# Kernel optimization log

Hardware: AMD Instinct MI355X
Metric: run time of the kernel (lower is better)

The kernel has to match this reference:

```python
import jax, jax.numpy as jnp
import numpy as np

NUM_HEADS = 16
NUM_BUCKETS = 32
MAX_DISTANCE = 128


def _rel_bucket(rel):
    # bidirectional T5-style relative position bucketing
    nb = NUM_BUCKETS // 2
    ret = (rel > 0).astype(jnp.int32) * nb
    n = jnp.abs(rel)
    max_exact = nb // 2
    is_small = n < max_exact
    safe = jnp.maximum(n, 1).astype(jnp.float32)
    large = max_exact + (jnp.log(safe / max_exact) / np.log(MAX_DISTANCE / max_exact) * (nb - max_exact)).astype(jnp.int32)
    large = jnp.minimum(large, nb - 1)
    return ret + jnp.where(is_small, n, large)


def setup_inputs() -> dict:
    key = jax.random.key(0)
    ks = jax.random.split(key, 12)
    S, B, E = 1024, 4, 1024
    D = E // NUM_HEADS
    s = 0.02
    return {
        "query": jax.random.normal(ks[0], (S, B, E), jnp.float32),
        "q_w": jax.random.normal(ks[1], (E, E), jnp.float32) * s,
        "q_b": jnp.zeros((E,), jnp.float32),
        "k_w": jax.random.normal(ks[2], (E, E), jnp.float32) * s,
        "k_b": jnp.zeros((E,), jnp.float32),
        "v_w": jax.random.normal(ks[3], (E, E), jnp.float32) * s,
        "v_b": jnp.zeros((E,), jnp.float32),
        "out_w": jax.random.normal(ks[4], (E, E), jnp.float32) * s,
        "out_b": jnp.zeros((E,), jnp.float32),
        "rel_emb": jax.random.normal(ks[5], (NUM_BUCKETS, NUM_HEADS), jnp.float32) * s,
        "grep_w": jax.random.normal(ks[6], (8, D), jnp.float32) * s,
        "grep_b": jnp.zeros((8,), jnp.float32),
        "grep_a": jnp.ones((NUM_HEADS,), jnp.float32),
    }


def reference(query, q_w, q_b, k_w, k_b, v_w, v_b, out_w, out_b, rel_emb, grep_w, grep_b, grep_a):
    S, B, E = query.shape
    H = NUM_HEADS
    D = E // H
    scaling = D ** -0.5

    q = (query @ q_w.T + q_b) * scaling  # scaling applied before gating, as in WavLM
    k = query @ k_w.T + k_b
    v = query @ v_w.T + v_b

    def split(x):  # (S,B,E) -> (B,H,S,D)
        return x.reshape(S, B, H, D).transpose(1, 2, 0, 3)

    q4, k4, v4 = split(q), split(k), split(v)

    attn = jnp.einsum('bhqd,bhkd->bhqk', q4, k4)  # (B,H,S,S)

    pos = jnp.arange(S)
    bucket = _rel_bucket(pos[None, :] - pos[:, None])  # (S,S)
    pbias = rel_emb[bucket].transpose(2, 0, 1)          # (H,S,S)

    # GRU-gated relative position scaling
    g = jnp.einsum('bhsd,ed->bhse', q4, grep_w) + grep_b      # (B,H,S,8)
    g = jax.nn.sigmoid(g.reshape(B, H, S, 2, 4).sum(-1))     # (B,H,S,2)
    gate_a, gate_b = g[..., 0], g[..., 1]
    gate = gate_a * (gate_b * grep_a[None, :, None] - 1.0) + 2.0  # (B,H,S)

    attn = attn + gate[..., None] * pbias[None]
    probs = jax.nn.softmax(attn, axis=-1)
    ctx = jnp.einsum('bhqk,bhkd->bhqd', probs, v4)  # (B,H,S,D)
    out = ctx.transpose(2, 0, 1, 3).reshape(S, B, E) @ out_w.T + out_b
    return out
```

## Files before the change

kernel.cpp:

```cpp
#include <hip/hip_runtime.h>
#include <stdint.h>


typedef short bf16x8 __attribute__((ext_vector_type(8)));
typedef float f32x4 __attribute__((ext_vector_type(4)));

#define MFMA_BF16(a, b, c) __builtin_amdgcn_mfma_f32_16x16x32_bf16((a), (b), (c), 0, 0, 0)

#define LOG2E 1.44269504088896f
#define LN2 0.693147180559945f

__device__ __forceinline__ unsigned short f2bf(float x) {
  union { float f; unsigned u; } v; v.f = x;
  unsigned r = v.u + 0x7fffu + ((v.u >> 16) & 1u);
  return (unsigned short)(r >> 16);
}
__device__ __forceinline__ float bf2f(unsigned short u) {
  union { unsigned u; float f; } v; v.u = ((unsigned)u) << 16;
  return v.f;
}

__device__ __forceinline__ void gload_lds16(const void* g, void* l) {
  __builtin_amdgcn_global_load_lds(
      (const __attribute__((address_space(1))) unsigned int*)g,
      (__attribute__((address_space(3))) unsigned int*)l, 16, 0, 0);
}

__device__ __forceinline__ int swz(int row) { return (row ^ (row >> 2)) & 3; }

__global__ __launch_bounds__(256) void prep_kernel(
    const float* __restrict__ query, const float* __restrict__ q_w,
    const float* __restrict__ k_w, const float* __restrict__ v_w,
    const float* __restrict__ out_w, const float* __restrict__ rel_emb,
    unsigned short* __restrict__ q_bf, unsigned short* __restrict__ wq,
    unsigned short* __restrict__ wk, unsigned short* __restrict__ wv,
    unsigned short* __restrict__ ohi, unsigned short* __restrict__ olo,
    float* __restrict__ bias_d) {
  int i = blockIdx.x * 256 + threadIdx.x;
  if (i < 4194304) {
    int e = i & 1023;
    int sb = i >> 10;
    int s = sb >> 2, b = sb & 3;
    q_bf[((size_t)(b * 1024 + s) << 10) | e] = f2bf(query[i]);
  } else if (i < 5242880) {
    int j = i - 4194304;
    wq[j] = f2bf(q_w[j]);
    wk[j] = f2bf(k_w[j]);
    wv[j] = f2bf(v_w[j]);
    float x = out_w[j];
    unsigned short h = f2bf(x);
    ohi[j] = h;
    olo[j] = f2bf(x - bf2f(h));
  } else {
    int idx = i - 5242880;
    if (idx >= 2048) return;
    if (idx == 2047) {
#pragma unroll
      for (int h = 0; h < 16; ++h) bias_d[h * 2048 + idx] = 0.f;
      return;
    }
    int rel = idx - 1023;
    int n = rel < 0 ? -rel : rel;
    int ret = rel > 0 ? 16 : 0;
    int bucket;
    if (n < 8) {
      bucket = ret + n;
    } else {
      int large = 8 + (int)(logf((float)n / 8.0f) / logf(16.0f) * 8.0f);
      if (large > 15) large = 15;
      bucket = ret + large;
    }
#pragma unroll
    for (int h = 0; h < 16; ++h)
      bias_d[h * 2048 + idx] = rel_emb[bucket * 16 + h] * LOG2E;
  }
}

__global__ __launch_bounds__(256, 3) void qkv_gemm_kernel(
    const unsigned short* __restrict__ A, const unsigned short* __restrict__ Wq,
    const unsigned short* __restrict__ Wk, const unsigned short* __restrict__ Wv,
    const float* __restrict__ qb, const float* __restrict__ kb, const float* __restrict__ vb,
    unsigned short* __restrict__ qh,
    unsigned short* __restrict__ kh,
    unsigned short* __restrict__ vT)
{
  __shared__ __align__(16) char smem[32768];
  const int tid = threadIdx.x, lane = tid & 63;
  const int wv_ = tid >> 6;
  const int nt = blockIdx.x;
  const int mt = blockIdx.y;
  const int mat = nt >> 3;
  const unsigned short* W = mat == 0 ? Wq : (mat == 1 ? Wk : Wv);
  const int n0 = (nt & 7) * 128;
  const int m0 = mt * 128;
  const int moff = (wv_ & 1) * 64;
  const int noff = (wv_ >> 1) * 64;

  f32x4 acc[4][4] = {};
  const char* Ab = (const char*)A;
  const char* Wb = (const char*)W;

  int st_row[2], st_g[2];
#pragma unroll
  for (int c = 0; c < 2; ++c) {
    int o = c * 4096 + tid * 16;
    int row = o >> 6, p = (o >> 4) & 3;
    st_row[c] = row;
    st_g[c] = p ^ swz(row);
  }

#define QKV_STAGE(kt, buf)                                                     \
  {                                                                            \
    char* bb = smem + (buf)*16384;                                             \
    _Pragma("unroll") for (int c = 0; c < 2; ++c) {                            \
      int o = c * 4096 + tid * 16;                                             \
      size_t ga = (size_t)(m0 + st_row[c]) * 2048 + (size_t)(kt)*64 + st_g[c] * 16; \
      size_t gb = (size_t)(n0 + st_row[c]) * 2048 + (size_t)(kt)*64 + st_g[c] * 16; \
      gload_lds16(Ab + ga, bb + o);                                            \
      gload_lds16(Wb + gb, bb + 8192 + o);                                     \
    }                                                                          \
  }

  QKV_STAGE(0, 0);
  for (int kt = 0; kt < 32; ++kt) {
    __syncthreads();
    const char* base = smem + (kt & 1) * 16384;
    if (kt < 31) QKV_STAGE(kt + 1, (kt + 1) & 1);

    bf16x8 af[4], bfr[4];
#pragma unroll
    for (int i = 0; i < 4; ++i) {
      int ra = moff + i * 16 + (lane & 15);
      int rb = noff + i * 16 + (lane & 15);
      int q = lane >> 4;
      af[i] = *(const bf16x8*)(base + ra * 64 + (q ^ swz(ra)) * 16);
      bfr[i] = *(const bf16x8*)(base + 8192 + rb * 64 + (q ^ swz(rb)) * 16);
    }
#pragma unroll
    for (int i = 0; i < 4; ++i)
#pragma unroll
      for (int j = 0; j < 4; ++j) acc[i][j] = MFMA_BF16(af[i], bfr[j], acc[i][j]);
  }
#undef QKV_STAGE

  const int bidx = m0 >> 10;
  const int s00 = (m0 & 1023) + moff + ((lane >> 4) << 2);
  const int c0 = n0 + noff + (lane & 15);
  if (mat < 2) {
    const float* barr = mat == 0 ? qb : kb;
    unsigned short* dst = mat == 0 ? qh : kh;
    const float scale = mat == 0 ? (0.125f * LOG2E) : 1.0f;
#pragma unroll
    for (int j = 0; j < 4; ++j) {
      int col = c0 + j * 16;
      int hh = col >> 6, dd = col & 63;
      float bias = barr[col];
#pragma unroll
      for (int i = 0; i < 4; ++i)
#pragma unroll
        for (int r = 0; r < 4; ++r) {
          int s = s00 + i * 16 + r;
          dst[((size_t)(bidx * 16 + hh) * 1024 + s) * 64 + dd] =
              f2bf((acc[i][j][r] + bias) * scale);
        }
    }
  } else {
#pragma unroll
    for (int j = 0; j < 4; ++j) {
      int col = c0 + j * 16;
      int hh = col >> 6, dd = col & 63;
      float bias = vb[col];
#pragma unroll
      for (int i = 0; i < 4; ++i) {
        int s = s00 + i * 16;
        ushort4 pk;
        pk.x = f2bf(acc[i][j][0] + bias);
        pk.y = f2bf(acc[i][j][1] + bias);
        pk.z = f2bf(acc[i][j][2] + bias);
        pk.w = f2bf(acc[i][j][3] + bias);
        *(ushort4*)&vT[((size_t)(bidx * 16 + hh) * 64 + dd) * 1024 + s] = pk;
      }
    }
  }
}

__global__ __launch_bounds__(256) void gate_kernel(const unsigned short* __restrict__ qh,
                                                   const float* __restrict__ grep_w,
                                                   const float* __restrict__ grep_b,
                                                   const float* __restrict__ grep_a,
                                                   float* __restrict__ gate) {
  __shared__ float gw[512];
  __shared__ float gbb[8];
  __shared__ float gaa[16];
  int tid = threadIdx.x;
  for (int i = tid; i < 512; i += 256) gw[i] = grep_w[i];
  if (tid < 8) gbb[tid] = grep_b[tid];
  if (tid < 16) gaa[tid] = grep_a[tid];
  __syncthreads();
  int idx = blockIdx.x * 256 + tid;
  int h = (idx >> 10) & 15;
  const unsigned short* qrow = qh + (size_t)idx * 64;
  float a[8] = {0.f, 0.f, 0.f, 0.f, 0.f, 0.f, 0.f, 0.f};
#pragma unroll
  for (int c = 0; c < 8; ++c) {
    bf16x8 v = *(const bf16x8*)(qrow + c * 8);
#pragma unroll
    for (int jj = 0; jj < 8; ++jj) {
      float qv = bf2f((unsigned short)v[jj]);
      int d = c * 8 + jj;
#pragma unroll
      for (int e = 0; e < 8; ++e) a[e] += qv * gw[e * 64 + d];
    }
  }
  float sa = (a[0] + a[1] + a[2] + a[3]) * LN2 + gbb[0] + gbb[1] + gbb[2] + gbb[3];
  float sb = (a[4] + a[5] + a[6] + a[7]) * LN2 + gbb[4] + gbb[5] + gbb[6] + gbb[7];
  float siga = 1.f / (1.f + __expf(-sa));
  float sigb = 1.f / (1.f + __expf(-sb));
  gate[idx] = siga * (sigb * gaa[h] - 1.f) + 2.f;
}

__global__ __launch_bounds__(512, 6) void attn_kernel(
    const unsigned short* __restrict__ qh, const unsigned short* __restrict__ kh,
    const unsigned short* __restrict__ vT, const float* __restrict__ gate,
    const float* __restrict__ bias_d, unsigned short* __restrict__ ctx_hi,
    unsigned short* __restrict__ ctx_lo) {
  __shared__ __align__(16) char smem[53760];
  const int tid = threadIdx.x, lane = tid & 63, w = tid >> 6;
  const int bh = blockIdx.x;
  const int h = bh & 15;
  const int s0 = blockIdx.y * 128;
  const int sqb = s0 + w * 16;
  const int q15 = lane & 15, quad = lane >> 4, q7 = lane & 7;

  float* biasw = (float*)(smem + 49152);
  if (tid < 288)
    ((float4*)biasw)[tid] = ((const float4*)(bias_d + h * 2048 + (896 - s0)))[tid];

  const char* kbase = (const char*)(kh + (size_t)bh * 65536);
  const char* vbase = (const char*)(vT + (size_t)bh * 65536);

  const int o = tid * 16;
  const int srow = o >> 7;
  const int sg = ((o >> 4) & 7) ^ (srow & 7);
  const size_t koff = (size_t)srow * 128 + sg * 16;
  const size_t voff = (size_t)srow * 2048 + sg * 16;

  gload_lds16(kbase + koff, smem + o);
  gload_lds16(vbase + voff, smem + 16384 + o);

  const unsigned short* qbase = qh + ((size_t)bh * 1024 + sqb + q15) * 64 + (quad << 3);
  bf16x8 qf0 = *(const bf16x8*)(qbase);
  bf16x8 qf1 = *(const bf16x8*)(qbase + 32);

  const int sq = sqb + q15;
  const float gate_lane = gate[bh * 1024 + sq];

  unsigned short* psrow = (unsigned short*)(smem + 32768 + w * 2048) + q15 * 64;

  float l_run = 0.f;
  f32x4 acc_o[4] = {};

  for (int kc = 0; kc < 16; ++kc) {
    __syncthreads();
    const char* Kc = smem + (kc & 1) * 8192;
    const char* Vc = smem + 16384 + (kc & 1) * 8192;
    if (kc < 15) {
      int nb = (kc + 1) & 1;
      gload_lds16(kbase + (size_t)(kc + 1) * 8192 + koff, smem + nb * 8192 + o);
      gload_lds16(vbase + (size_t)(kc + 1) * 128 + voff, smem + 16384 + nb * 8192 + o);
    }

    const int boff = kc * 64 - sq + s0 + 127 + (quad << 2);
    float ps = 0.f;
#pragma unroll
    for (int t = 0; t < 4; ++t) {
      f32x4 sacc = {};
      int key = t * 16 + q15;
#pragma unroll
      for (int dc = 0; dc < 2; ++dc) {
        int c16 = dc * 4 + quad;
        bf16x8 ak = *(const bf16x8*)(Kc + key * 128 + ((c16 ^ (key & 7)) << 4));
        sacc = MFMA_BF16(ak, dc ? qf1 : qf0, sacc);
      }
      float p0 = __builtin_exp2f(__builtin_fmaf(gate_lane, biasw[boff + t * 16 + 0], sacc[0]));
      float p1 = __builtin_exp2f(__builtin_fmaf(gate_lane, biasw[boff + t * 16 + 1], sacc[1]));
      float p2 = __builtin_exp2f(__builtin_fmaf(gate_lane, biasw[boff + t * 16 + 2], sacc[2]));
      float p3 = __builtin_exp2f(__builtin_fmaf(gate_lane, biasw[boff + t * 16 + 3], sacc[3]));
      ps += (p0 + p1) + (p2 + p3);
      ushort4 pk;
      pk.x = f2bf(p0); pk.y = f2bf(p1); pk.z = f2bf(p2); pk.w = f2bf(p3);
      int c = t * 4 + quad;
      int pc = (c >> 1) ^ q7;
      *(ushort4*)(psrow + pc * 8 + (c & 1) * 4) = pk;
    }
    l_run += ps;

#pragma unroll
    for (int ch = 0; ch < 2; ++ch) {
      int j = (ch * 4 + quad) ^ q7;
      bf16x8 pb = *(const bf16x8*)(psrow + j * 8);
#pragma unroll
      for (int t = 0; t < 4; ++t) {
        int d = t * 16 + q15;
        int c16 = ch * 4 + quad;
        bf16x8 av = *(const bf16x8*)(Vc + d * 128 + ((c16 ^ (d & 7)) << 4));
        acc_o[t] = MFMA_BF16(av, pb, acc_o[t]);
      }
    }
  }

  l_run += __shfl_xor(l_run, 16, 64);
  l_run += __shfl_xor(l_run, 32, 64);
  const float inv = 1.0f / l_run;

  __syncthreads();
  float* Ot = (float*)smem;
  {
    float* ow = Ot + (w * 16 + q15) * 65;
#pragma unroll
    for (int t = 0; t < 4; ++t)
#pragma unroll
      for (int r = 0; r < 4; ++r) ow[t * 16 + (quad << 2) + r] = acc_o[t][r] * inv;
  }
  __syncthreads();
  {
    int row = tid >> 2, dg = tid & 3;
    int s = s0 + row;
    const float* src = Ot + row * 65 + dg * 16;
    unsigned short hibuf[16], lobuf[16];
#pragma unroll
    for (int j = 0; j < 16; ++j) {
      float v = src[j];
      unsigned short hu = f2bf(v);
      hibuf[j] = hu;
      lobuf[j] = f2bf(v - bf2f(hu));
    }
    size_t base = (size_t)(s * 4 + (bh >> 4)) * 1024 + h * 64 + dg * 16;
#pragma unroll
    for (int half = 0; half < 2; ++half) {
      *(uint4*)(ctx_hi + base + half * 8) = *(const uint4*)(hibuf + half * 8);
      *(uint4*)(ctx_lo + base + half * 8) = *(const uint4*)(lobuf + half * 8);
    }
  }
}

__global__ __launch_bounds__(256, 3) void outproj_kernel(
    const unsigned short* __restrict__ Ahi, const unsigned short* __restrict__ Alo,
    const unsigned short* __restrict__ Bhi, const unsigned short* __restrict__ Blo,
    const float* __restrict__ ob, float* __restrict__ out) {
  __shared__ __align__(16) char smem[49152];
  const int tid = threadIdx.x, lane = tid & 63, wv_ = tid >> 6;
  const int q15 = lane & 15, quad = lane >> 4;
  const int n0 = blockIdx.x * 128;
  const int m0 = blockIdx.y * 64;
  const int moff = (wv_ & 1) * 32;
  const int noff = (wv_ >> 1) * 64;

  const int oa = tid * 16;
  const int ra_ = oa >> 6;
  const int ga_ = (((oa >> 4) & 3) ^ swz(ra_)) << 4;
  int rb_[2], gb_[2], obo_[2];
#pragma unroll
  for (int c = 0; c < 2; ++c) {
    int ob2 = c * 4096 + tid * 16;
    obo_[c] = ob2;
    rb_[c] = ob2 >> 6;
    gb_[c] = (((ob2 >> 4) & 3) ^ swz(rb_[c])) << 4;
  }

#define OP_STAGE(kt, buf)                                                        \
  {                                                                              \
    char* bb = smem + (buf)*24576;                                               \
    size_t ga = (size_t)(m0 + ra_) * 2048 + (size_t)(kt)*64 + ga_;               \
    gload_lds16((const char*)Ahi + ga, bb + oa);                                 \
    gload_lds16((const char*)Alo + ga, bb + 4096 + oa);                          \
    _Pragma("unroll") for (int c = 0; c < 2; ++c) {                              \
      size_t gb = (size_t)(n0 + rb_[c]) * 2048 + (size_t)(kt)*64 + gb_[c];       \
      gload_lds16((const char*)Bhi + gb, bb + 8192 + obo_[c]);                   \
      gload_lds16((const char*)Blo + gb, bb + 16384 + obo_[c]);                  \
    }                                                                            \
  }

  f32x4 acc[2][4] = {};
  OP_STAGE(0, 0);
  for (int kt = 0; kt < 32; ++kt) {
    __syncthreads();
    const char* base = smem + (kt & 1) * 24576;
    if (kt < 31) OP_STAGE(kt + 1, (kt + 1) & 1);

    bf16x8 ah[2], al[2], bhf[4], blf[4];
#pragma unroll
    for (int i = 0; i < 2; ++i) {
      int ra = moff + i * 16 + q15;
      int pa = (quad ^ swz(ra)) << 4;
      ah[i] = *(const bf16x8*)(base + ra * 64 + pa);
      al[i] = *(const bf16x8*)(base + 4096 + ra * 64 + pa);
    }
#pragma unroll
    for (int j = 0; j < 4; ++j) {
      int rb = noff + j * 16 + q15;
      int pb = (quad ^ swz(rb)) << 4;
      bhf[j] = *(const bf16x8*)(base + 8192 + rb * 64 + pb);
      blf[j] = *(const bf16x8*)(base + 16384 + rb * 64 + pb);
    }
#pragma unroll
    for (int i = 0; i < 2; ++i)
#pragma unroll
      for (int j = 0; j < 4; ++j) {
        f32x4 t = MFMA_BF16(al[i], bhf[j], acc[i][j]);
        t = MFMA_BF16(ah[i], blf[j], t);
        acc[i][j] = MFMA_BF16(ah[i], bhf[j], t);
      }
  }
#undef OP_STAGE

  const int rr0 = m0 + moff + (quad << 2);
  const int c0 = n0 + noff + q15;
#pragma unroll
  for (int j = 0; j < 4; ++j) {
    int col = c0 + j * 16;
    float bias = ob[col];
#pragma unroll
    for (int i = 0; i < 2; ++i)
#pragma unroll
      for (int r = 0; r < 4; ++r)
        out[(size_t)(rr0 + i * 16 + r) * 1024 + col] = acc[i][j][r] + bias;
  }
}

extern "C" void kernel_launch(void* const* d_in, const int* in_sizes, int n_in,
                              void* d_out, int out_size, void* d_ws, size_t ws_size,
                              hipStream_t stream) {
  const float* query = (const float*)d_in[0];
  const float* q_w = (const float*)d_in[1];
  const float* q_b = (const float*)d_in[2];
  const float* k_w = (const float*)d_in[3];
  const float* k_b = (const float*)d_in[4];
  const float* v_w = (const float*)d_in[5];
  const float* v_b = (const float*)d_in[6];
  const float* out_w = (const float*)d_in[7];
  const float* out_b = (const float*)d_in[8];
  const float* rel_emb = (const float*)d_in[9];
  const float* grep_w = (const float*)d_in[10];
  const float* grep_b = (const float*)d_in[11];
  const float* grep_a = (const float*)d_in[12];
  float* out = (float*)d_out;

  const size_t MB = 1u << 20;
  char* ws = (char*)d_ws;
  unsigned short* q_bf = (unsigned short*)(ws);
  unsigned short* wq_bf = (unsigned short*)(ws + 8 * MB);
  unsigned short* wk_bf = (unsigned short*)(ws + 10 * MB);
  unsigned short* wv_bf = (unsigned short*)(ws + 12 * MB);
  unsigned short* ow_hi = (unsigned short*)(ws + 14 * MB);
  unsigned short* ow_lo = (unsigned short*)(ws + 16 * MB);
  unsigned short* qhp = (unsigned short*)(ws + 18 * MB);
  unsigned short* khp = (unsigned short*)(ws + 26 * MB);
  unsigned short* vTp = (unsigned short*)(ws + 34 * MB);
  unsigned short* ctxh = (unsigned short*)(ws + 42 * MB);
  unsigned short* ctxl = (unsigned short*)(ws + 50 * MB);
  float* gatep = (float*)(ws + 58 * MB);
  float* biasp = (float*)(ws + 58 * MB + 256 * 1024);

  prep_kernel<<<20488, 256, 0, stream>>>(query, q_w, k_w, v_w, out_w, rel_emb, q_bf, wq_bf,
                                         wk_bf, wv_bf, ow_hi, ow_lo, biasp);
  qkv_gemm_kernel<<<dim3(24, 32), 256, 0, stream>>>(q_bf, wq_bf, wk_bf, wv_bf, q_b, k_b, v_b,
                                                    qhp, khp, vTp);
  gate_kernel<<<256, 256, 0, stream>>>(qhp, grep_w, grep_b, grep_a, gatep);
  attn_kernel<<<dim3(64, 8), 512, 0, stream>>>(qhp, khp, vTp, gatep, biasp, ctxh, ctxl);
  outproj_kernel<<<dim3(8, 64), 256, 0, stream>>>(ctxh, ctxl, ow_hi, ow_lo, out_b, out);
}
```

Measured before the change: 211.4 us.

## Use fp16 single-pass out-projection and 32x32 MFMA attention with bf16 bias

The out-projection drops the hi/lo bf16 split (three MFMAs per tile) in favor of a single fp16 MFMA on fp16 context and weights, which halves LDS and global traffic for that GEMM. The attention kernel moves to 256-thread blocks with 32x32x16 MFMAs, where each wave handles 32 query rows. The relative bias is stored as bf16 in two parity-shifted LDS copies so it can be read as packed 32-bit pairs. This trades numerical precision in the output projection and bias for fewer instructions and less memory traffic, and occupancy may change.

```diff
diff --git a/kernel.cpp b/kernel.cpp
--- a/kernel.cpp
+++ b/kernel.cpp
@@ -3,9 +3,13 @@
 
 
 typedef short bf16x8 __attribute__((ext_vector_type(8)));
+typedef _Float16 f16x8 __attribute__((ext_vector_type(8)));
 typedef float f32x4 __attribute__((ext_vector_type(4)));
+typedef float f32x16 __attribute__((ext_vector_type(16)));
 
 #define MFMA_BF16(a, b, c) __builtin_amdgcn_mfma_f32_16x16x32_bf16((a), (b), (c), 0, 0, 0)
+#define MFMA_F16(a, b, c) __builtin_amdgcn_mfma_f32_16x16x32_f16((a), (b), (c), 0, 0, 0)
+#define MFMA32_BF16(a, b, c) __builtin_amdgcn_mfma_f32_32x32x16_bf16((a), (b), (c), 0, 0, 0)
 
 #define LOG2E 1.44269504088896f
 #define LN2 0.693147180559945f
@@ -17,6 +21,18 @@
 }
 __device__ __forceinline__ float bf2f(unsigned short u) {
   union { unsigned u; float f; } v; v.u = ((unsigned)u) << 16;
+  return v.f;
+}
+__device__ __forceinline__ unsigned short f2h(float x) {
+  union { _Float16 h; unsigned short u; } v; v.h = (_Float16)x;
+  return v.u;
+}
+__device__ __forceinline__ float u32lo_bf(unsigned u) {
+  union { unsigned u; float f; } v; v.u = u << 16;
+  return v.f;
+}
+__device__ __forceinline__ float u32hi_bf(unsigned u) {
+  union { unsigned u; float f; } v; v.u = u & 0xffff0000u;
   return v.f;
 }
 
@@ -34,8 +50,8 @@
     const float* __restrict__ out_w, const float* __restrict__ rel_emb,
     unsigned short* __restrict__ q_bf, unsigned short* __restrict__ wq,
     unsigned short* __restrict__ wk, unsigned short* __restrict__ wv,
-    unsigned short* __restrict__ ohi, unsigned short* __restrict__ olo,
-    float* __restrict__ bias_d) {
+    unsigned short* __restrict__ ow_h,
+    unsigned short* __restrict__ bias_hd) {
   int i = blockIdx.x * 256 + threadIdx.x;
   if (i < 4194304) {
     int e = i & 1023;
@@ -47,16 +63,13 @@
     wq[j] = f2bf(q_w[j]);
     wk[j] = f2bf(k_w[j]);
     wv[j] = f2bf(v_w[j]);
-    float x = out_w[j];
-    unsigned short h = f2bf(x);
-    ohi[j] = h;
-    olo[j] = f2bf(x - bf2f(h));
+    ow_h[j] = f2h(out_w[j]);
   } else {
     int idx = i - 5242880;
-    if (idx >= 2048) return;
-    if (idx == 2047) {
-#pragma unroll
-      for (int h = 0; h < 16; ++h) bias_d[h * 2048 + idx] = 0.f;
+    if (idx >= 2056) return;
+    if (idx >= 2047) {
+#pragma unroll
+      for (int h = 0; h < 16; ++h) bias_hd[h * 2056 + idx] = 0;
       return;
     }
     int rel = idx - 1023;
@@ -72,7 +85,7 @@
     }
 #pragma unroll
     for (int h = 0; h < 16; ++h)
-      bias_d[h * 2048 + idx] = rel_emb[bucket * 16 + h] * LOG2E;
+      bias_hd[h * 2056 + idx] = f2bf(rel_emb[bucket * 16 + h] * LOG2E);
   }
 }
 
@@ -219,46 +232,58 @@
   gate[idx] = siga * (sigb * gaa[h] - 1.f) + 2.f;
 }
 
-__global__ __launch_bounds__(512, 6) void attn_kernel(
+__global__ __launch_bounds__(256, 2) void attn_kernel(
     const unsigned short* __restrict__ qh, const unsigned short* __restrict__ kh,
     const unsigned short* __restrict__ vT, const float* __restrict__ gate,
-    const float* __restrict__ bias_d, unsigned short* __restrict__ ctx_hi,
-    unsigned short* __restrict__ ctx_lo) {
-  __shared__ __align__(16) char smem[53760];
+    const unsigned short* __restrict__ bias_hd, unsigned short* __restrict__ ctx) {
+  __shared__ __align__(16) char smem[55808];
   const int tid = threadIdx.x, lane = tid & 63, w = tid >> 6;
   const int bh = blockIdx.x;
   const int h = bh & 15;
-  const int s0 = blockIdx.y * 128;
-  const int sqb = s0 + w * 16;
-  const int q15 = lane & 15, quad = lane >> 4, q7 = lane & 7;
-
-  float* biasw = (float*)(smem + 49152);
-  if (tid < 288)
-    ((float4*)biasw)[tid] = ((const float4*)(bias_d + h * 2048 + (896 - s0)))[tid];
+  const int qs0 = blockIdx.y * 128;
+  const int q31 = lane & 31, hb = lane >> 5, q7 = q31 & 7;
+  const int sq = qs0 + w * 32 + q31;
+
+  unsigned short* bc0 = (unsigned short*)(smem + 51200);
+  unsigned short* bc1 = (unsigned short*)(smem + 53504);
+  {
+    const unsigned short* gb = bias_hd + h * 2056 + (896 - qs0);
+    for (int i = tid; i < 1152; i += 256) {
+      bc0[i] = gb[i];
+      bc1[i] = gb[i + 1];
+    }
+  }
 
   const char* kbase = (const char*)(kh + (size_t)bh * 65536);
   const char* vbase = (const char*)(vT + (size_t)bh * 65536);
 
-  const int o = tid * 16;
-  const int srow = o >> 7;
-  const int sg = ((o >> 4) & 7) ^ (srow & 7);
-  const size_t koff = (size_t)srow * 128 + sg * 16;
-  const size_t voff = (size_t)srow * 2048 + sg * 16;
-
-  gload_lds16(kbase + koff, smem + o);
-  gload_lds16(vbase + voff, smem + 16384 + o);
-
-  const unsigned short* qbase = qh + ((size_t)bh * 1024 + sqb + q15) * 64 + (quad << 3);
-  bf16x8 qf0 = *(const bf16x8*)(qbase);
-  bf16x8 qf1 = *(const bf16x8*)(qbase + 32);
-
-  const int sq = sqb + q15;
+  const int o1 = tid * 16, o2 = o1 + 4096;
+  const int r1 = o1 >> 7, r2 = o2 >> 7;
+  const int g1 = ((o1 >> 4) & 7) ^ (r1 & 7);
+  const int g2 = ((o2 >> 4) & 7) ^ (r2 & 7);
+  const size_t k1 = (size_t)r1 * 128 + g1 * 16, k2 = (size_t)r2 * 128 + g2 * 16;
+  const size_t v1 = (size_t)r1 * 2048 + g1 * 16, v2 = (size_t)r2 * 2048 + g2 * 16;
+
+  gload_lds16(kbase + k1, smem + o1);
+  gload_lds16(kbase + k2, smem + o2);
+  gload_lds16(vbase + v1, smem + 16384 + o1);
+  gload_lds16(vbase + v2, smem + 16384 + o2);
+
+  const unsigned short* qrow = qh + ((size_t)bh * 1024 + sq) * 64 + hb * 8;
+  bf16x8 qf[4];
+#pragma unroll
+  for (int dc = 0; dc < 4; ++dc) qf[dc] = *(const bf16x8*)(qrow + dc * 16);
+
   const float gate_lane = gate[bh * 1024 + sq];
 
-  unsigned short* psrow = (unsigned short*)(smem + 32768 + w * 2048) + q15 * 64;
+  const int par = (127 - w * 32 - q31) & 1;
+  const unsigned int* bp = (const unsigned int*)(par ? bc1 : bc0);
+  const int bbase0 = (qs0 + 127 - sq - par) >> 1;
+
+  char* psrow = smem + 32768 + (w * 32 + q31) * 144;
 
   float l_run = 0.f;
-  f32x4 acc_o[4] = {};
+  f32x16 accO0 = {}, accO1 = {};
 
   for (int kc = 0; kc < 16; ++kc) {
     __syncthreads();
@@ -266,89 +291,93 @@
     const char* Vc = smem + 16384 + (kc & 1) * 8192;
     if (kc < 15) {
       int nb = (kc + 1) & 1;
-      gload_lds16(kbase + (size_t)(kc + 1) * 8192 + koff, smem + nb * 8192 + o);
-      gload_lds16(vbase + (size_t)(kc + 1) * 128 + voff, smem + 16384 + nb * 8192 + o);
-    }
-
-    const int boff = kc * 64 - sq + s0 + 127 + (quad << 2);
+      gload_lds16(kbase + (size_t)(kc + 1) * 8192 + k1, smem + nb * 8192 + o1);
+      gload_lds16(kbase + (size_t)(kc + 1) * 8192 + k2, smem + nb * 8192 + o2);
+      gload_lds16(vbase + (size_t)(kc + 1) * 128 + v1, smem + 16384 + nb * 8192 + o1);
+      gload_lds16(vbase + (size_t)(kc + 1) * 128 + v2, smem + 16384 + nb * 8192 + o2);
+    }
+
+    f32x16 sacA = {}, sacB = {};
+#pragma unroll
+    for (int ks = 0; ks < 4; ++ks) {
+      int ch = ((ks * 2 + hb) ^ q7) << 4;
+      bf16x8 k0 = *(const bf16x8*)(Kc + q31 * 128 + ch);
+      bf16x8 kk1 = *(const bf16x8*)(Kc + (32 + q31) * 128 + ch);
+      sacA = MFMA32_BF16(k0, qf[ks], sacA);
+      sacB = MFMA32_BF16(kk1, qf[ks], sacB);
+    }
+
     float ps = 0.f;
 #pragma unroll
-    for (int t = 0; t < 4; ++t) {
-      f32x4 sacc = {};
-      int key = t * 16 + q15;
-#pragma unroll
-      for (int dc = 0; dc < 2; ++dc) {
-        int c16 = dc * 4 + quad;
-        bf16x8 ak = *(const bf16x8*)(Kc + key * 128 + ((c16 ^ (key & 7)) << 4));
-        sacc = MFMA_BF16(ak, dc ? qf1 : qf0, sacc);
+    for (int kt = 0; kt < 2; ++kt) {
+#pragma unroll
+      for (int rg = 0; rg < 4; ++rg) {
+        int runoff = kt * 32 + rg * 8 + hb * 4;
+        int idx = bbase0 + ((kc * 64 + runoff) >> 1);
+        unsigned int u0 = bp[idx], u1 = bp[idx + 1];
+        float s0v = (kt ? sacB : sacA)[rg * 4 + 0];
+        float s1v = (kt ? sacB : sacA)[rg * 4 + 1];
+        float s2v = (kt ? sacB : sacA)[rg * 4 + 2];
+        float s3v = (kt ? sacB : sacA)[rg * 4 + 3];
+        float p0 = __builtin_exp2f(__builtin_fmaf(gate_lane, u32lo_bf(u0), s0v));
+        float p1 = __builtin_exp2f(__builtin_fmaf(gate_lane, u32hi_bf(u0), s1v));
+        float p2 = __builtin_exp2f(__builtin_fmaf(gate_lane, u32lo_bf(u1), s2v));
+        float p3 = __builtin_exp2f(__builtin_fmaf(gate_lane, u32hi_bf(u1), s3v));
+        ps += (p0 + p1) + (p2 + p3);
+        ushort4 pk;
+        pk.x = f2bf(p0); pk.y = f2bf(p1); pk.z = f2bf(p2); pk.w = f2bf(p3);
+        int c = kt * 4 + rg;
+        *(ushort4*)(psrow + ((c ^ q7) << 4) + hb * 8) = pk;
       }
-      float p0 = __builtin_exp2f(__builtin_fmaf(gate_lane, biasw[boff + t * 16 + 0], sacc[0]));
-      float p1 = __builtin_exp2f(__builtin_fmaf(gate_lane, biasw[boff + t * 16 + 1], sacc[1]));
-      float p2 = __builtin_exp2f(__builtin_fmaf(gate_lane, biasw[boff + t * 16 + 2], sacc[2]));
-      float p3 = __builtin_exp2f(__builtin_fmaf(gate_lane, biasw[boff + t * 16 + 3], sacc[3]));
-      ps += (p0 + p1) + (p2 + p3);
-      ushort4 pk;
-      pk.x = f2bf(p0); pk.y = f2bf(p1); pk.z = f2bf(p2); pk.w = f2bf(p3);
-      int c = t * 4 + quad;
-      int pc = (c >> 1) ^ q7;
-      *(ushort4*)(psrow + pc * 8 + (c & 1) * 4) = pk;
     }
     l_run += ps;
 
 #pragma unroll
-    for (int ch = 0; ch < 2; ++ch) {
-      int j = (ch * 4 + quad) ^ q7;
-      bf16x8 pb = *(const bf16x8*)(psrow + j * 8);
-#pragma unroll
-      for (int t = 0; t < 4; ++t) {
-        int d = t * 16 + q15;
-        int c16 = ch * 4 + quad;
-        bf16x8 av = *(const bf16x8*)(Vc + d * 128 + ((c16 ^ (d & 7)) << 4));
-        acc_o[t] = MFMA_BF16(av, pb, acc_o[t]);
-      }
-    }
-  }
-
-  l_run += __shfl_xor(l_run, 16, 64);
+    for (int ks = 0; ks < 4; ++ks) {
+      int cc = (ks * 2 + hb) ^ q7;
+      bf16x8 pb = *(const bf16x8*)(psrow + (cc << 4));
+      int ch = cc << 4;
+      bf16x8 v0f = *(const bf16x8*)(Vc + q31 * 128 + ch);
+      bf16x8 v1f = *(const bf16x8*)(Vc + (32 + q31) * 128 + ch);
+      accO0 = MFMA32_BF16(v0f, pb, accO0);
+      accO1 = MFMA32_BF16(v1f, pb, accO1);
+    }
+  }
+
   l_run += __shfl_xor(l_run, 32, 64);
   const float inv = 1.0f / l_run;
 
   __syncthreads();
   float* Ot = (float*)smem;
   {
-    float* ow = Ot + (w * 16 + q15) * 65;
-#pragma unroll
-    for (int t = 0; t < 4; ++t)
-#pragma unroll
-      for (int r = 0; r < 4; ++r) ow[t * 16 + (quad << 2) + r] = acc_o[t][r] * inv;
+    float* ow = Ot + (w * 32 + q31) * 68;
+#pragma unroll
+    for (int rr = 0; rr < 16; ++rr) {
+      int d = (rr & 3) + 8 * (rr >> 2) + 4 * hb;
+      ow[d] = accO0[rr] * inv;
+      ow[32 + d] = accO1[rr] * inv;
+    }
   }
   __syncthreads();
   {
-    int row = tid >> 2, dg = tid & 3;
-    int s = s0 + row;
-    const float* src = Ot + row * 65 + dg * 16;
-    unsigned short hibuf[16], lobuf[16];
-#pragma unroll
-    for (int j = 0; j < 16; ++j) {
-      float v = src[j];
-      unsigned short hu = f2bf(v);
-      hibuf[j] = hu;
-      lobuf[j] = f2bf(v - bf2f(hu));
-    }
-    size_t base = (size_t)(s * 4 + (bh >> 4)) * 1024 + h * 64 + dg * 16;
-#pragma unroll
-    for (int half = 0; half < 2; ++half) {
-      *(uint4*)(ctx_hi + base + half * 8) = *(const uint4*)(hibuf + half * 8);
-      *(uint4*)(ctx_lo + base + half * 8) = *(const uint4*)(lobuf + half * 8);
-    }
+    int row = tid >> 1, dg = tid & 1;
+    int s = qs0 + row;
+    const float* src = Ot + row * 68 + dg * 32;
+    unsigned short hbuf[32];
+#pragma unroll
+    for (int j = 0; j < 32; ++j) hbuf[j] = f2h(src[j]);
+    size_t base = (size_t)(s * 4 + (bh >> 4)) * 1024 + h * 64 + dg * 32;
+#pragma unroll
+    for (int qd = 0; qd < 4; ++qd)
+      *(uint4*)(ctx + base + qd * 8) = *(const uint4*)(hbuf + qd * 8);
   }
 }
 
 __global__ __launch_bounds__(256, 3) void outproj_kernel(
-    const unsigned short* __restrict__ Ahi, const unsigned short* __restrict__ Alo,
-    const unsigned short* __restrict__ Bhi, const unsigned short* __restrict__ Blo,
+    const unsigned short* __restrict__ Af,
+    const unsigned short* __restrict__ Bf,
     const float* __restrict__ ob, float* __restrict__ out) {
-  __shared__ __align__(16) char smem[49152];
+  __shared__ __align__(16) char smem[24576];
   const int tid = threadIdx.x, lane = tid & 63, wv_ = tid >> 6;
   const int q15 = lane & 15, quad = lane >> 4;
   const int n0 = blockIdx.x * 128;
@@ -370,14 +399,12 @@
 
 #define OP_STAGE(kt, buf)                                                        \
   {                                                                              \
-    char* bb = smem + (buf)*24576;                                               \
+    char* bb = smem + (buf)*12288;                                               \
     size_t ga = (size_t)(m0 + ra_) * 2048 + (size_t)(kt)*64 + ga_;               \
-    gload_lds16((const char*)Ahi + ga, bb + oa);                                 \
-    gload_lds16((const char*)Alo + ga, bb + 4096 + oa);                          \
+    gload_lds16((const char*)Af + ga, bb + oa);                                  \
     _Pragma("unroll") for (int c = 0; c < 2; ++c) {                              \
       size_t gb = (size_t)(n0 + rb_[c]) * 2048 + (size_t)(kt)*64 + gb_[c];       \
-      gload_lds16((const char*)Bhi + gb, bb + 8192 + obo_[c]);                   \
-      gload_lds16((const char*)Blo + gb, bb + 16384 + obo_[c]);                  \
+      gload_lds16((const char*)Bf + gb, bb + 4096 + obo_[c]);                    \
     }                                                                            \
   }
 
@@ -385,32 +412,24 @@
   OP_STAGE(0, 0);
   for (int kt = 0; kt < 32; ++kt) {
     __syncthreads();
-    const char* base = smem + (kt & 1) * 24576;
+    const char* base = smem + (kt & 1) * 12288;
     if (kt < 31) OP_STAGE(kt + 1, (kt + 1) & 1);
 
-    bf16x8 ah[2], al[2], bhf[4], blf[4];
+    f16x8 ah[2], bhf[4];
 #pragma unroll
     for (int i = 0; i < 2; ++i) {
       int ra = moff + i * 16 + q15;
-      int pa = (quad ^ swz(ra)) << 4;
-      ah[i] = *(const bf16x8*)(base + ra * 64 + pa);
-      al[i] = *(const bf16x8*)(base + 4096 + ra * 64 + pa);
+      ah[i] = *(const f16x8*)(base + ra * 64 + ((quad ^ swz(ra)) << 4));
     }
 #pragma unroll
     for (int j = 0; j < 4; ++j) {
       int rb = noff + j * 16 + q15;
-      int pb = (quad ^ swz(rb)) << 4;
-      bhf[j] = *(const bf16x8*)(base + 8192 + rb * 64 + pb);
-      blf[j] = *(const bf16x8*)(base + 16384 + rb * 64 + pb);
+      bhf[j] = *(const f16x8*)(base + 4096 + rb * 64 + ((quad ^ swz(rb)) << 4));
     }
 #pragma unroll
     for (int i = 0; i < 2; ++i)
 #pragma unroll
-      for (int j = 0; j < 4; ++j) {
-        f32x4 t = MFMA_BF16(al[i], bhf[j], acc[i][j]);
-        t = MFMA_BF16(ah[i], blf[j], t);
-        acc[i][j] = MFMA_BF16(ah[i], bhf[j], t);
-      }
+      for (int j = 0; j < 4; ++j) acc[i][j] = MFMA_F16(ah[i], bhf[j], acc[i][j]);
   }
 #undef OP_STAGE
 
@@ -452,21 +471,19 @@
   unsigned short* wq_bf = (unsigned short*)(ws + 8 * MB);
   unsigned short* wk_bf = (unsigned short*)(ws + 10 * MB);
   unsigned short* wv_bf = (unsigned short*)(ws + 12 * MB);
-  unsigned short* ow_hi = (unsigned short*)(ws + 14 * MB);
-  unsigned short* ow_lo = (unsigned short*)(ws + 16 * MB);
-  unsigned short* qhp = (unsigned short*)(ws + 18 * MB);
-  unsigned short* khp = (unsigned short*)(ws + 26 * MB);
-  unsigned short* vTp = (unsigned short*)(ws + 34 * MB);
-  unsigned short* ctxh = (unsigned short*)(ws + 42 * MB);
-  unsigned short* ctxl = (unsigned short*)(ws + 50 * MB);
-  float* gatep = (float*)(ws + 58 * MB);
-  float* biasp = (float*)(ws + 58 * MB + 256 * 1024);
-
-  prep_kernel<<<20488, 256, 0, stream>>>(query, q_w, k_w, v_w, out_w, rel_emb, q_bf, wq_bf,
-                                         wk_bf, wv_bf, ow_hi, ow_lo, biasp);
+  unsigned short* ow_h = (unsigned short*)(ws + 14 * MB);
+  unsigned short* qhp = (unsigned short*)(ws + 16 * MB);
+  unsigned short* khp = (unsigned short*)(ws + 24 * MB);
+  unsigned short* vTp = (unsigned short*)(ws + 32 * MB);
+  unsigned short* ctxp = (unsigned short*)(ws + 40 * MB);
+  float* gatep = (float*)(ws + 48 * MB);
+  unsigned short* biasp = (unsigned short*)(ws + 48 * MB + 256 * 1024);
+
+  prep_kernel<<<20489, 256, 0, stream>>>(query, q_w, k_w, v_w, out_w, rel_emb, q_bf, wq_bf,
+                                         wk_bf, wv_bf, ow_h, biasp);
   qkv_gemm_kernel<<<dim3(24, 32), 256, 0, stream>>>(q_bf, wq_bf, wk_bf, wv_bf, q_b, k_b, v_b,
                                                     qhp, khp, vTp);
   gate_kernel<<<256, 256, 0, stream>>>(qhp, grep_w, grep_b, grep_a, gatep);
-  attn_kernel<<<dim3(64, 8), 512, 0, stream>>>(qhp, khp, vTp, gatep, biasp, ctxh, ctxl);
-  outproj_kernel<<<dim3(8, 64), 256, 0, stream>>>(ctxh, ctxl, ow_hi, ow_lo, out_b, out);
-}
+  attn_kernel<<<dim3(64, 8), 256, 0, stream>>>(qhp, khp, vTp, gatep, biasp, ctxp);
+  outproj_kernel<<<dim3(8, 64), 256, 0, stream>>>(ctxp, ow_h, out_b, out);
+}
```

Result: faster. 206.9 us (-2.1%).
